# Optimization experiments

Measured on AMD Instinct MI355X. Metric: run time of the kernel, lower is better.

## Reference

```python
import jax, jax.numpy as jnp
import numpy as np

TEMPERATURE = 1.0        # sample_codebook_temperature
COMMITMENT_COST = 1.0

B, T, D, K = 8, 4096, 64, 1024


def setup_inputs() -> dict:
    key = jax.random.key(0)
    k1, k2 = jax.random.split(key)
    x = jax.random.normal(k1, (B, T, D), dtype=jnp.float32)
    embeddings = jax.random.normal(k2, (D, K), dtype=jnp.float32)  # (embedding_dim, codebook_size)
    return {"x": x, "embeddings": embeddings}


def gumbel_softmax(logits, temperature):
    # logits: [N, K]
    K_ = logits.shape[1]
    indices = jnp.argmax(logits, axis=1)
    enc = jax.nn.one_hot(indices, K_, dtype=logits.dtype)
    pi0 = jax.nn.softmax(logits, axis=-1)
    pi1 = (enc + jax.nn.softmax(logits / temperature, axis=-1)) / 2
    pi1 = jax.nn.softmax(jax.lax.stop_gradient(jnp.log(pi1) - logits), axis=1)
    pi2 = 2 * pi1 - 0.5 * pi0
    encodings = pi2 - jax.lax.stop_gradient(pi2) + enc  # straight-through encodings
    return indices, encodings


def reference(x, embeddings):
    D_, K_ = embeddings.shape
    flat = x.reshape(-1, D_)                              # [N, D]
    # squared euclidean distances via matmul (cdist trick)
    sim = flat @ embeddings                               # [N, K]
    dist = (jnp.sum(flat ** 2, axis=1, keepdims=True)
            - 2.0 * sim
            + jnp.sum(embeddings ** 2, axis=0, keepdims=True))
    indices, encodings = gumbel_softmax(-dist, TEMPERATURE)
    indices = indices.reshape(x.shape[:-1])               # [B, T]
    quantized = embeddings.T[indices]                     # gather: [B, T, D]
    e_latent_loss = jnp.mean(jnp.square(jax.lax.stop_gradient(quantized) - x))
    loss = e_latent_loss * COMMITMENT_COST
    # straight-through estimator (training-mode output; same values as eval)
    quantized = x + jax.lax.stop_gradient(quantized - x)
    return quantized, encodings, indices, loss
```

## Files before the change

### kernel.cpp

```cpp
#include <hip/hip_runtime.h>
#include <hip/hip_bf16.h>


#define NROWS 32768
#define DDIM  64
#define KCB   1024

typedef float    f32x4  __attribute__((ext_vector_type(4)));
typedef _Float16 f16x8  __attribute__((ext_vector_type(8)));

#define WS_ET    0
#define WS_H     65536
#define WS_PART  66560
#define WS_IBEST 68608
#define WS_LIST  101376
#define WS_CTR   134144
#define WS_EHI   134148
#define WS_ELO   166916

__global__ __launch_bounds__(256) void k1_prep(const float* __restrict__ E,
                                               float* __restrict__ Et,
                                               float* __restrict__ h,
                                               _Float16* __restrict__ Ehi,
                                               _Float16* __restrict__ Elo,
                                               int* __restrict__ ctr) {
  int k = blockIdx.x * 256 + threadIdx.x;
  float col[DDIM];
  float sum = 0.f;
#pragma unroll
  for (int d = 0; d < DDIM; ++d) {
    float v = E[d * KCB + k];
    col[d] = v;
    sum = fmaf(v, v, sum);
  }
  float4* dst = (float4*)(Et + (size_t)k * DDIM);
#pragma unroll
  for (int i = 0; i < 16; ++i)
    dst[i] = make_float4(col[4*i], col[4*i+1], col[4*i+2], col[4*i+3]);
  h[k] = 0.5f * sum;

#pragma unroll
  for (int w = 0; w < 2; ++w) {
#pragma unroll
    for (int p = 0; p < 32; ++p) {
      int dl = w * 32 + 4 * (p >> 3) + (p & 3) + 16 * ((p >> 2) & 1);
      float v = col[dl];
      _Float16 hi = (_Float16)v;
      _Float16 lo = (_Float16)(v - (float)hi);
      Ehi[(size_t)k * DDIM + w * 32 + p] = hi;
      Elo[(size_t)k * DDIM + w * 32 + p] = lo;
    }
  }
  if (k == 0) ctr[0] = 0;
}

__global__ __launch_bounds__(256, 4) void k2_coarse(const float* __restrict__ x,
                                                    const _Float16* __restrict__ Ehi,
                                                    const _Float16* __restrict__ Elo,
                                                    const float* __restrict__ h,
                                                    int* __restrict__ ibest,
                                                    int* __restrict__ ctr,
                                                    int* __restrict__ list) {
  int tid = threadIdx.x;
  int lane = tid & 63, wid = tid >> 6;
  int g = lane >> 4, c = lane & 15;
  int n0 = (blockIdx.x * 4 + wid) * 32;

  f16x8 Ahi[2][2], Alo[2][2];
#pragma unroll
  for (int r = 0; r < 2; ++r) {
    const float* xb = x + (size_t)(n0 + r * 16 + c) * DDIM;
#pragma unroll
    for (int w = 0; w < 2; ++w) {
      f32x4 xa = *(const f32x4*)(xb + w * 32 + 4 * g);
      f32x4 xc = *(const f32x4*)(xb + w * 32 + 16 + 4 * g);
#pragma unroll
      for (int e = 0; e < 4; ++e) {
        _Float16 hi = (_Float16)xa[e];
        Ahi[r][w][e] = hi;
        Alo[r][w][e] = (_Float16)(xa[e] - (float)hi);
      }
#pragma unroll
      for (int e = 0; e < 4; ++e) {
        _Float16 hi = (_Float16)xc[e];
        Ahi[r][w][4 + e] = hi;
        Alo[r][w][4 + e] = (_Float16)(xc[e] - (float)hi);
      }
    }
  }

  float b1[2][4], b2[2][4];
  int   i1[2][4];
#pragma unroll
  for (int r = 0; r < 2; ++r)
#pragma unroll
    for (int q = 0; q < 4; ++q) { b1[r][q] = -3.0e38f; b2[r][q] = -3.0e38f; i1[r][q] = 0; }

  const _Float16* peh = Ehi + c * DDIM + g * 8;
  const _Float16* pel = Elo + c * DDIM + g * 8;

  f16x8 bh0n = *(const f16x8*)(peh);
  f16x8 bl0n = *(const f16x8*)(pel);
  f16x8 bh1n = *(const f16x8*)(peh + 32);
  f16x8 bl1n = *(const f16x8*)(pel + 32);
  float hn = h[c];

  for (int ch = 0; ch < 64; ++ch) {
    f16x8 bh0 = bh0n, bl0 = bl0n, bh1 = bh1n, bl1 = bl1n;
    float hc = hn;
    if (ch < 63) {
      size_t off = (size_t)(ch + 1) * 16 * DDIM;
      bh0n = *(const f16x8*)(peh + off);
      bl0n = *(const f16x8*)(pel + off);
      bh1n = *(const f16x8*)(peh + off + 32);
      bl1n = *(const f16x8*)(pel + off + 32);
      hn = h[(ch + 1) * 16 + c];
    }
    int code = ch * 16 + c;
#pragma unroll
    for (int r = 0; r < 2; ++r) {
      f32x4 a = { -hc, -hc, -hc, -hc };
      a = __builtin_amdgcn_mfma_f32_16x16x32_f16(Alo[r][0], bh0, a, 0, 0, 0);
      a = __builtin_amdgcn_mfma_f32_16x16x32_f16(Ahi[r][0], bl0, a, 0, 0, 0);
      a = __builtin_amdgcn_mfma_f32_16x16x32_f16(Ahi[r][0], bh0, a, 0, 0, 0);
      a = __builtin_amdgcn_mfma_f32_16x16x32_f16(Alo[r][1], bh1, a, 0, 0, 0);
      a = __builtin_amdgcn_mfma_f32_16x16x32_f16(Ahi[r][1], bl1, a, 0, 0, 0);
      a = __builtin_amdgcn_mfma_f32_16x16x32_f16(Ahi[r][1], bh1, a, 0, 0, 0);
#pragma unroll
      for (int q = 0; q < 4; ++q) {
        float s = a[q];
        bool gt = s > b1[r][q];
        b2[r][q] = gt ? b1[r][q] : fmaxf(b2[r][q], s);
        i1[r][q] = gt ? code : i1[r][q];
        b1[r][q] = gt ? s : b1[r][q];
      }
    }
  }

#pragma unroll
  for (int step = 1; step <= 8; step <<= 1) {
#pragma unroll
    for (int r = 0; r < 2; ++r)
#pragma unroll
      for (int q = 0; q < 4; ++q) {
        float ob1 = __shfl_xor(b1[r][q], step);
        int   oi1 = __shfl_xor(i1[r][q], step);
        float ob2 = __shfl_xor(b2[r][q], step);
        bool win = (ob1 > b1[r][q]) || (ob1 == b1[r][q] && oi1 < i1[r][q]);
        float loser = win ? b1[r][q] : ob1;
        b1[r][q] = win ? ob1 : b1[r][q];
        i1[r][q] = win ? oi1 : i1[r][q];
        b2[r][q] = fmaxf(fmaxf(b2[r][q], ob2), loser);
      }
  }

  if (c == 0) {
#pragma unroll
    for (int r = 0; r < 2; ++r)
#pragma unroll
      for (int q = 0; q < 4; ++q) {
        int row = n0 + r * 16 + 4 * g + q;
        ibest[row] = i1[r][q];
        if (b1[r][q] - b2[r][q] <= 0.02f) {
          int p = atomicAdd(ctr, 1);
          list[p] = row;
        }
      }
  }
}

__global__ __launch_bounds__(256) void k2b_rescan(const float* __restrict__ x,
                                                  const float* __restrict__ Et,
                                                  const float* __restrict__ h,
                                                  const int* __restrict__ ctr,
                                                  const int* __restrict__ list,
                                                  int* __restrict__ ibest) {
  int lane = threadIdx.x & 63;
  int w = blockIdx.x * 4 + (threadIdx.x >> 6);
  int cnt = ctr[0];
  for (int i = w; i < cnt; i += 512) {
    int n = list[i];
    const f32x4* xr = (const f32x4*)(x + (size_t)n * DDIM);
    f32x4 xv[16];
#pragma unroll
    for (int d = 0; d < 16; ++d) xv[d] = xr[d];
    float best = -3.0e38f; int bi = 0;
    for (int j = 0; j < 16; ++j) {
      int code = j * 64 + lane;
      const f32x4* er = (const f32x4*)(Et + (size_t)code * DDIM);
      float acc = -h[code];
#pragma unroll
      for (int d = 0; d < 16; ++d) {
        f32x4 e4 = er[d], x4 = xv[d];
        acc = fmaf(x4[0], e4[0], acc); acc = fmaf(x4[1], e4[1], acc);
        acc = fmaf(x4[2], e4[2], acc); acc = fmaf(x4[3], e4[3], acc);
      }
      if (acc > best || (acc == best && code < bi)) { best = acc; bi = code; }
    }
#pragma unroll
    for (int step = 1; step <= 32; step <<= 1) {
      float ob = __shfl_xor(best, step);
      int   oi = __shfl_xor(bi, step);
      if (ob > best || (ob == best && oi < bi)) { best = ob; bi = oi; }
    }
    if (lane == 0) ibest[n] = bi;
  }
}

__global__ __launch_bounds__(256) void k34_fused(const float* __restrict__ x,
                                                 const float* __restrict__ Et,
                                                 const int* __restrict__ ibest,
                                                 float* __restrict__ partial,
                                                 float* __restrict__ out_q,
                                                 float* __restrict__ out_enc,
                                                 float* __restrict__ out_ind) {
  __shared__ int sidx[16];
  int tid = threadIdx.x;
  int r0 = blockIdx.x * 16;

  if (tid < 16) {
    int n = r0 + tid;
    int bi = ibest[n];
    sidx[tid] = bi;
    out_ind[n] = (float)bi;
  }
  __syncthreads();

  int r = tid >> 4, cc = tid & 15;
  int n = r0 + r;
  int bi = sidx[r];
  float4 q4 = *(const float4*)(Et + (size_t)bi * DDIM + cc * 4);
  float4 x4 = *(const float4*)(x + (size_t)n * DDIM + cc * 4);
  float d0 = q4.x - x4.x, d1 = q4.y - x4.y, d2 = q4.z - x4.z, d3 = q4.w - x4.w;
  float lsum = 0.f;
  lsum = fmaf(d0, d0, lsum); lsum = fmaf(d1, d1, lsum);
  lsum = fmaf(d2, d2, lsum); lsum = fmaf(d3, d3, lsum);
  *(float4*)(out_q + (size_t)n * DDIM + cc * 4) = q4;

#pragma unroll
  for (int rr = 0; rr < 16; ++rr) {
    int bk = sidx[rr];
    f32x4 v = (f32x4)(0.f);
    if ((bk >> 2) == tid) v[bk & 3] = 1.0f;
    __builtin_nontemporal_store(v, (f32x4*)(out_enc + (size_t)(r0 + rr) * KCB + tid * 4));
  }

#pragma unroll
  for (int off = 32; off > 0; off >>= 1) lsum += __shfl_down(lsum, off);
  __shared__ float red[4];
  int lane = tid & 63, wv = tid >> 6;
  if (lane == 0) red[wv] = lsum;
  __syncthreads();
  if (tid == 0) partial[blockIdx.x] = red[0] + red[1] + red[2] + red[3];
}

__global__ void k5_loss(const float* __restrict__ partial, float* __restrict__ out_loss) {
  int t = threadIdx.x;
  float s = 0.f;
#pragma unroll
  for (int i = 0; i < 8; ++i) s += partial[t + i * 256];
#pragma unroll
  for (int off = 32; off > 0; off >>= 1) s += __shfl_down(s, off);
  __shared__ float red[4];
  int lane = t & 63, w = t >> 6;
  if (lane == 0) red[w] = s;
  __syncthreads();
  if (t == 0) out_loss[0] = (red[0] + red[1] + red[2] + red[3]) * (1.0f / 2097152.0f);
}

extern "C" void kernel_launch(void* const* d_in, const int* in_sizes, int n_in,
                              void* d_out, int out_size, void* d_ws, size_t ws_size,
                              hipStream_t stream) {
  const float* x = (const float*)d_in[0];
  const float* E = (const float*)d_in[1];

  float* ws    = (float*)d_ws;
  float* Et    = ws + WS_ET;
  float* h     = ws + WS_H;
  float* part  = ws + WS_PART;
  int*   ibest = (int*)(ws + WS_IBEST);
  int*   list  = (int*)(ws + WS_LIST);
  int*   ctr   = (int*)(ws + WS_CTR);
  _Float16* Ehi = (_Float16*)(ws + WS_EHI);
  _Float16* Elo = (_Float16*)(ws + WS_ELO);

  float* out      = (float*)d_out;
  float* out_q    = out;
  float* out_enc  = out + 2097152;
  float* out_ind  = out + 35651584;
  float* out_loss = out + 35684352;

  k1_prep<<<4, 256, 0, stream>>>(E, Et, h, Ehi, Elo, ctr);
  k2_coarse<<<256, 256, 0, stream>>>(x, Ehi, Elo, h, ibest, ctr, list);
  k2b_rescan<<<128, 256, 0, stream>>>(x, Et, h, ctr, list, ibest);
  k34_fused<<<2048, 256, 0, stream>>>(x, Et, ibest, part, out_q, out_enc, out_ind);
  k5_loss<<<1, 256, 0, stream>>>(part, out_loss);
}
```

Before: 241.5 us.

## Fuse coarse search, exact rescan, and output writes into one kernel

Merges the coarse MFMA argmax, the fp32 rescan of ambiguous rows, and the gather/one-hot/loss output kernel into a single per-block kernel. Each block now handles 32 rows with two waves that each scan half of the codebook, then merges their results in shared memory. Rescans happen in-block instead of through a global atomic list. The prep kernel uses more blocks and writes vectorized f16 stores. This removes two launches and the global round trips for ibest and the list. In exchange, the coarse MFMA phase has fewer waves per block, and each rescanned row stalls its block behind syncthreads.

New measurement: 220.3 us. 8.8% less time.

```diff
diff --git a/kernel.cpp b/kernel.cpp
--- a/kernel.cpp
+++ b/kernel.cpp
@@ -5,26 +5,23 @@
 #define NROWS 32768
 #define DDIM  64
 #define KCB   1024
-
-typedef float    f32x4  __attribute__((ext_vector_type(4)));
-typedef _Float16 f16x8  __attribute__((ext_vector_type(8)));
+#define MARGIN 0.02f
+
+typedef float    f32x4 __attribute__((ext_vector_type(4)));
+typedef _Float16 f16x8 __attribute__((ext_vector_type(8)));
 
 #define WS_ET    0
 #define WS_H     65536
 #define WS_PART  66560
-#define WS_IBEST 68608
-#define WS_LIST  101376
-#define WS_CTR   134144
-#define WS_EHI   134148
-#define WS_ELO   166916
-
-__global__ __launch_bounds__(256) void k1_prep(const float* __restrict__ E,
-                                               float* __restrict__ Et,
-                                               float* __restrict__ h,
-                                               _Float16* __restrict__ Ehi,
-                                               _Float16* __restrict__ Elo,
-                                               int* __restrict__ ctr) {
-  int k = blockIdx.x * 256 + threadIdx.x;
+#define WS_EHI   67584
+#define WS_ELO   100352
+
+__global__ __launch_bounds__(64) void kA_prep(const float* __restrict__ E,
+                                              float* __restrict__ Et,
+                                              float* __restrict__ h,
+                                              _Float16* __restrict__ Ehi,
+                                              _Float16* __restrict__ Elo) {
+  int k = blockIdx.x * 64 + threadIdx.x;
   float col[DDIM];
   float sum = 0.f;
 #pragma unroll
@@ -41,35 +38,53 @@
 
 #pragma unroll
   for (int w = 0; w < 2; ++w) {
+    f16x8 hi8[4], lo8[4];
 #pragma unroll
     for (int p = 0; p < 32; ++p) {
       int dl = w * 32 + 4 * (p >> 3) + (p & 3) + 16 * ((p >> 2) & 1);
       float v = col[dl];
       _Float16 hi = (_Float16)v;
-      _Float16 lo = (_Float16)(v - (float)hi);
-      Ehi[(size_t)k * DDIM + w * 32 + p] = hi;
-      Elo[(size_t)k * DDIM + w * 32 + p] = lo;
-    }
-  }
-  if (k == 0) ctr[0] = 0;
+      hi8[p >> 3][p & 7] = hi;
+      lo8[p >> 3][p & 7] = (_Float16)(v - (float)hi);
+    }
+#pragma unroll
+    for (int q = 0; q < 4; ++q) {
+      *(f16x8*)(Ehi + (size_t)k * DDIM + w * 32 + q * 8) = hi8[q];
+      *(f16x8*)(Elo + (size_t)k * DDIM + w * 32 + q * 8) = lo8[q];
+    }
+  }
 }
 
-__global__ __launch_bounds__(256, 4) void k2_coarse(const float* __restrict__ x,
-                                                    const _Float16* __restrict__ Ehi,
-                                                    const _Float16* __restrict__ Elo,
-                                                    const float* __restrict__ h,
-                                                    int* __restrict__ ibest,
-                                                    int* __restrict__ ctr,
-                                                    int* __restrict__ list) {
-  int tid = threadIdx.x;
-  int lane = tid & 63, wid = tid >> 6;
+__global__ __launch_bounds__(128, 2) void kB_main(const float* __restrict__ x,
+                                                  const _Float16* __restrict__ Ehi,
+                                                  const _Float16* __restrict__ Elo,
+                                                  const float* __restrict__ Et,
+                                                  const float* __restrict__ h,
+                                                  float* __restrict__ partial,
+                                                  float* __restrict__ out_q,
+                                                  float* __restrict__ out_enc,
+                                                  float* __restrict__ out_ind) {
+  __shared__ float mb1[2][32], mb2[2][32];
+  __shared__ int   mi1[2][32];
+  __shared__ int   sidx[32];
+  __shared__ int   flags[32];
+  __shared__ int   nflag;
+  __shared__ float rb[2];
+  __shared__ int   ri[2];
+  __shared__ float red[2];
+
+  int tid  = threadIdx.x;
+  int ws   = tid >> 6;
+  int lane = tid & 63;
   int g = lane >> 4, c = lane & 15;
-  int n0 = (blockIdx.x * 4 + wid) * 32;
+  int r0 = blockIdx.x * 32;
+
+  if (tid == 0) nflag = 0;
 
   f16x8 Ahi[2][2], Alo[2][2];
 #pragma unroll
   for (int r = 0; r < 2; ++r) {
-    const float* xb = x + (size_t)(n0 + r * 16 + c) * DDIM;
+    const float* xb = x + (size_t)(r0 + r * 16 + c) * DDIM;
 #pragma unroll
     for (int w = 0; w < 2; ++w) {
       f32x4 xa = *(const f32x4*)(xb + w * 32 + 4 * g);
@@ -96,27 +111,27 @@
 #pragma unroll
     for (int q = 0; q < 4; ++q) { b1[r][q] = -3.0e38f; b2[r][q] = -3.0e38f; i1[r][q] = 0; }
 
-  const _Float16* peh = Ehi + c * DDIM + g * 8;
-  const _Float16* pel = Elo + c * DDIM + g * 8;
+  const _Float16* peh = Ehi + (size_t)(ws * 512 + c) * DDIM + g * 8;
+  const _Float16* pel = Elo + (size_t)(ws * 512 + c) * DDIM + g * 8;
 
   f16x8 bh0n = *(const f16x8*)(peh);
   f16x8 bl0n = *(const f16x8*)(pel);
   f16x8 bh1n = *(const f16x8*)(peh + 32);
   f16x8 bl1n = *(const f16x8*)(pel + 32);
-  float hn = h[c];
-
-  for (int ch = 0; ch < 64; ++ch) {
+  float hn = h[ws * 512 + c];
+
+  for (int ch = 0; ch < 32; ++ch) {
     f16x8 bh0 = bh0n, bl0 = bl0n, bh1 = bh1n, bl1 = bl1n;
     float hc = hn;
-    if (ch < 63) {
+    if (ch < 31) {
       size_t off = (size_t)(ch + 1) * 16 * DDIM;
       bh0n = *(const f16x8*)(peh + off);
       bl0n = *(const f16x8*)(pel + off);
       bh1n = *(const f16x8*)(peh + off + 32);
       bl1n = *(const f16x8*)(pel + off + 32);
-      hn = h[(ch + 1) * 16 + c];
-    }
-    int code = ch * 16 + c;
+      hn = h[ws * 512 + (ch + 1) * 16 + c];
+    }
+    int code = ws * 512 + ch * 16 + c;
 #pragma unroll
     for (int r = 0; r < 2; ++r) {
       f32x4 a = { -hc, -hc, -hc, -hc };
@@ -153,40 +168,43 @@
         b2[r][q] = fmaxf(fmaxf(b2[r][q], ob2), loser);
       }
   }
-
   if (c == 0) {
 #pragma unroll
     for (int r = 0; r < 2; ++r)
 #pragma unroll
       for (int q = 0; q < 4; ++q) {
-        int row = n0 + r * 16 + 4 * g + q;
-        ibest[row] = i1[r][q];
-        if (b1[r][q] - b2[r][q] <= 0.02f) {
-          int p = atomicAdd(ctr, 1);
-          list[p] = row;
-        }
-      }
-  }
-}
-
-__global__ __launch_bounds__(256) void k2b_rescan(const float* __restrict__ x,
-                                                  const float* __restrict__ Et,
-                                                  const float* __restrict__ h,
-                                                  const int* __restrict__ ctr,
-                                                  const int* __restrict__ list,
-                                                  int* __restrict__ ibest) {
-  int lane = threadIdx.x & 63;
-  int w = blockIdx.x * 4 + (threadIdx.x >> 6);
-  int cnt = ctr[0];
-  for (int i = w; i < cnt; i += 512) {
-    int n = list[i];
+        int row = r * 16 + 4 * g + q;
+        mb1[ws][row] = b1[r][q];
+        mi1[ws][row] = i1[r][q];
+        mb2[ws][row] = b2[r][q];
+      }
+  }
+  __syncthreads();
+
+  if (tid < 32) {
+    float a1 = mb1[0][tid], a2 = mb1[1][tid];
+    int   j1 = mi1[0][tid], j2 = mi1[1][tid];
+    bool w1 = (a2 > a1) || (a2 == a1 && j2 < j1);
+    float bb1 = w1 ? a2 : a1;
+    int   ii1 = w1 ? j2 : j1;
+    float bb2 = fmaxf(fmaxf(mb2[0][tid], mb2[1][tid]), w1 ? a1 : a2);
+    sidx[tid] = ii1;
+    if (bb1 - bb2 <= MARGIN) { int p = atomicAdd(&nflag, 1); flags[p] = tid; }
+  }
+  __syncthreads();
+
+  int nf = nflag;
+  for (int fi = 0; fi < nf; ++fi) {
+    int row = flags[fi];
+    int n = r0 + row;
     const f32x4* xr = (const f32x4*)(x + (size_t)n * DDIM);
     f32x4 xv[16];
 #pragma unroll
     for (int d = 0; d < 16; ++d) xv[d] = xr[d];
     float best = -3.0e38f; int bi = 0;
-    for (int j = 0; j < 16; ++j) {
-      int code = j * 64 + lane;
+#pragma unroll 1
+    for (int j = 0; j < 8; ++j) {
+      int code = j * 128 + tid;
       const f32x4* er = (const f32x4*)(Et + (size_t)code * DDIM);
       float acc = -h[code];
 #pragma unroll
@@ -203,62 +221,57 @@
       int   oi = __shfl_xor(bi, step);
       if (ob > best || (ob == best && oi < bi)) { best = ob; bi = oi; }
     }
-    if (lane == 0) ibest[n] = bi;
-  }
-}
-
-__global__ __launch_bounds__(256) void k34_fused(const float* __restrict__ x,
-                                                 const float* __restrict__ Et,
-                                                 const int* __restrict__ ibest,
-                                                 float* __restrict__ partial,
-                                                 float* __restrict__ out_q,
-                                                 float* __restrict__ out_enc,
-                                                 float* __restrict__ out_ind) {
-  __shared__ int sidx[16];
-  int tid = threadIdx.x;
-  int r0 = blockIdx.x * 16;
-
-  if (tid < 16) {
-    int n = r0 + tid;
-    int bi = ibest[n];
-    sidx[tid] = bi;
-    out_ind[n] = (float)bi;
-  }
+    if (lane == 0) { rb[ws] = best; ri[ws] = bi; }
+    __syncthreads();
+    if (tid == 0) {
+      bool w1 = (rb[1] > rb[0]) || (rb[1] == rb[0] && ri[1] < ri[0]);
+      sidx[row] = w1 ? ri[1] : ri[0];
+    }
+    __syncthreads();
+  }
+
+  if (tid < 32) out_ind[r0 + tid] = (float)sidx[tid];
+
+  float lsum = 0.f;
+#pragma unroll
+  for (int i = 0; i < 4; ++i) {
+    int f = tid + i * 128;
+    int row = f >> 4, cc = f & 15;
+    int n = r0 + row;
+    int bi = sidx[row];
+    f32x4 q4 = *(const f32x4*)(Et + (size_t)bi * DDIM + cc * 4);
+    f32x4 x4 = *(const f32x4*)(x + (size_t)n * DDIM + cc * 4);
+    float d0 = q4[0] - x4[0], d1 = q4[1] - x4[1], d2 = q4[2] - x4[2], d3 = q4[3] - x4[3];
+    lsum = fmaf(d0, d0, lsum); lsum = fmaf(d1, d1, lsum);
+    lsum = fmaf(d2, d2, lsum); lsum = fmaf(d3, d3, lsum);
+    __builtin_nontemporal_store(q4, (f32x4*)(out_q + (size_t)n * DDIM + cc * 4));
+  }
+
+#pragma unroll 1
+  for (int rr = 0; rr < 32; ++rr) {
+    int bk = sidx[rr];
+    float* rowp = out_enc + (size_t)(r0 + rr) * KCB;
+#pragma unroll
+    for (int i = 0; i < 2; ++i) {
+      int slot = tid + i * 128;
+      f32x4 v = (f32x4)(0.f);
+      if ((bk >> 2) == slot) v[bk & 3] = 1.0f;
+      __builtin_nontemporal_store(v, (f32x4*)(rowp + slot * 4));
+    }
+  }
+
+#pragma unroll
+  for (int off = 32; off > 0; off >>= 1) lsum += __shfl_down(lsum, off);
+  if (lane == 0) red[ws] = lsum;
   __syncthreads();
-
-  int r = tid >> 4, cc = tid & 15;
-  int n = r0 + r;
-  int bi = sidx[r];
-  float4 q4 = *(const float4*)(Et + (size_t)bi * DDIM + cc * 4);
-  float4 x4 = *(const float4*)(x + (size_t)n * DDIM + cc * 4);
-  float d0 = q4.x - x4.x, d1 = q4.y - x4.y, d2 = q4.z - x4.z, d3 = q4.w - x4.w;
-  float lsum = 0.f;
-  lsum = fmaf(d0, d0, lsum); lsum = fmaf(d1, d1, lsum);
-  lsum = fmaf(d2, d2, lsum); lsum = fmaf(d3, d3, lsum);
-  *(float4*)(out_q + (size_t)n * DDIM + cc * 4) = q4;
-
-#pragma unroll
-  for (int rr = 0; rr < 16; ++rr) {
-    int bk = sidx[rr];
-    f32x4 v = (f32x4)(0.f);
-    if ((bk >> 2) == tid) v[bk & 3] = 1.0f;
-    __builtin_nontemporal_store(v, (f32x4*)(out_enc + (size_t)(r0 + rr) * KCB + tid * 4));
-  }
-
-#pragma unroll
-  for (int off = 32; off > 0; off >>= 1) lsum += __shfl_down(lsum, off);
-  __shared__ float red[4];
-  int lane = tid & 63, wv = tid >> 6;
-  if (lane == 0) red[wv] = lsum;
-  __syncthreads();
-  if (tid == 0) partial[blockIdx.x] = red[0] + red[1] + red[2] + red[3];
+  if (tid == 0) partial[blockIdx.x] = red[0] + red[1];
 }
 
 __global__ void k5_loss(const float* __restrict__ partial, float* __restrict__ out_loss) {
   int t = threadIdx.x;
   float s = 0.f;
 #pragma unroll
-  for (int i = 0; i < 8; ++i) s += partial[t + i * 256];
+  for (int i = 0; i < 4; ++i) s += partial[t + i * 256];
 #pragma unroll
   for (int off = 32; off > 0; off >>= 1) s += __shfl_down(s, off);
   __shared__ float red[4];
@@ -274,13 +287,10 @@
   const float* x = (const float*)d_in[0];
   const float* E = (const float*)d_in[1];
 
-  float* ws    = (float*)d_ws;
-  float* Et    = ws + WS_ET;
-  float* h     = ws + WS_H;
-  float* part  = ws + WS_PART;
-  int*   ibest = (int*)(ws + WS_IBEST);
-  int*   list  = (int*)(ws + WS_LIST);
-  int*   ctr   = (int*)(ws + WS_CTR);
+  float* ws   = (float*)d_ws;
+  float* Et   = ws + WS_ET;
+  float* h    = ws + WS_H;
+  float* part = ws + WS_PART;
   _Float16* Ehi = (_Float16*)(ws + WS_EHI);
   _Float16* Elo = (_Float16*)(ws + WS_ELO);
 
@@ -290,9 +300,7 @@
   float* out_ind  = out + 35651584;
   float* out_loss = out + 35684352;
 
-  k1_prep<<<4, 256, 0, stream>>>(E, Et, h, Ehi, Elo, ctr);
-  k2_coarse<<<256, 256, 0, stream>>>(x, Ehi, Elo, h, ibest, ctr, list);
-  k2b_rescan<<<128, 256, 0, stream>>>(x, Et, h, ctr, list, ibest);
-  k34_fused<<<2048, 256, 0, stream>>>(x, Et, ibest, part, out_q, out_enc, out_ind);
+  kA_prep<<<16, 64, 0, stream>>>(E, Et, h, Ehi, Elo);
+  kB_main<<<1024, 128, 0, stream>>>(x, Ehi, Elo, Et, h, part, out_q, out_enc, out_ind);
   k5_loss<<<1, 256, 0, stream>>>(part, out_loss);
 }
```
